# Kernel tuning notes

Measured on AMD Instinct MI355X. Metric: run time of the kernel, lower is better.

The kernel has to match this reference:

```python
import jax, jax.numpy as jnp
import numpy as np

PS = 4          # patch_size (square)
STRIDE = 2
PAD = (PS - 1) // 2
HEADS = 8
DIM = 256       # attn_dim == dim (kv_dim > dim, dim_reduc=1)
KV_DIM = 512
HD = DIM // HEADS
SCALE = HD ** -0.5
NP2 = PS * PS   # 16 elements per window


def _unfold(x, k, s, p):
    """torch.nn.functional.unfold: (B,C,H,W) -> (B, C*k*k, Ho*Wo)."""
    B, C, H, W = x.shape
    xp = jnp.pad(x, ((0, 0), (0, 0), (p, p), (p, p)))
    Ho = (H + 2 * p - k) // s + 1
    Wo = (W + 2 * p - k) // s + 1
    r = (jnp.arange(Ho) * s)[:, None] + jnp.arange(k)   # (Ho,k)
    c = (jnp.arange(Wo) * s)[:, None] + jnp.arange(k)   # (Wo,k)
    pt = xp[:, :, r][:, :, :, :, c]                     # (B,C,Ho,k,Wo,k)
    pt = pt.transpose(0, 1, 3, 5, 2, 4)                 # (B,C,k,k,Ho,Wo)
    return pt.reshape(B, C * k * k, Ho * Wo)


def _fold(y, C, Hout, Wout, k, s, p):
    """torch.nn.functional.fold: (B, C*k*k, Ho*Wo) -> (B,C,Hout,Wout), overlap-add."""
    B = y.shape[0]
    Ho = (Hout + 2 * p - k) // s + 1
    Wo = (Wout + 2 * p - k) // s + 1
    pt = y.reshape(B, C, k, k, Ho, Wo).transpose(0, 1, 4, 2, 5, 3)  # (B,C,Ho,k,Wo,k)
    r = (jnp.arange(Ho) * s)[:, None] + jnp.arange(k)
    c = (jnp.arange(Wo) * s)[:, None] + jnp.arange(k)
    out = jnp.zeros((B, C, Hout + 2 * p, Wout + 2 * p), y.dtype)
    out = out.at[:, :, r[:, :, None, None], c[None, None, :, :]].add(pt)
    return out[:, :, p:Hout + p, p:Wout + p]


def _patch_softmax(attn, Ht, Wt, Hb, Wb):
    """Normalize exp(attn) by per-bottom-pixel sums computed via a fold/unfold round trip
    (faithful to the original, including its reshape layout)."""
    a = jnp.exp(attn)                                                # (B*HtWt, H, 16, 1)
    s = a.reshape(-1, Ht * Wt, HEADS, NP2).transpose(0, 2, 3, 1)     # (B, H, 16, HtWt)
    s = s.reshape(-1, NP2, Ht * Wt)                                  # (B*H, 16, HtWt)
    s = _fold(s, 1, Hb, Wb, PS, STRIDE, PAD)                         # (B*H, 1, Hb, Wb)
    s = _unfold(s, PS, STRIDE, PAD).transpose(0, 2, 1)               # (B*H, HtWt, 16)
    s = jnp.where(s == 0, jnp.ones((), s.dtype), s)
    return a / s.reshape(-1, HEADS, NP2, 1)


def _forward(Xt, Xb, q_w, kv_w, proj_w, proj_b, rel_init, rel_bias, Ht, Wt, Hb, Wb):
    B, _, C = Xb.shape
    # im2col: gather 4x4 windows of the fine map, one window per coarse token
    Xbp = Xb.transpose(0, 2, 1).reshape(B, C, Hb, Wb)
    Xbp = _unfold(Xbp, PS, STRIDE, PAD)                              # (B, C*16, Ht*Wt)
    Xbp = Xbp.reshape(B, C, NP2, Ht * Wt).transpose(0, 3, 2, 1)
    Xbp = Xbp.reshape(B * Ht * Wt, NP2, C)                           # queries (top_down)
    Xtq = Xt.reshape(-1, 1, Xt.shape[-1])                            # (B*HtWt, 1, kv_dim)

    q = (Xbp @ q_w.T).reshape(-1, NP2, HEADS, HD).transpose(0, 2, 1, 3)  # (BHW,H,16,hd)
    kv = (Xtq @ kv_w.T).reshape(-1, 1, 2, HEADS, HD).transpose(2, 0, 3, 1, 4)
    k, v = kv[0], kv[1]                                              # (BHW,H,1,hd)

    attn = (q @ jnp.swapaxes(k, -2, -1)) * SCALE                     # (BHW,H,16,1)
    attn = attn + rel_init[:, None] + rel_bias[:, None]
    attn = _patch_softmax(attn, Ht, Wt, Hb, Wb)

    out = (attn @ v).transpose(0, 2, 1, 3).reshape(-1, NP2, DIM)     # (BHW,16,DIM)
    out = out.reshape(B, Ht * Wt, NP2, DIM).transpose(0, 3, 2, 1)
    out = out.reshape(B, DIM * NP2, Ht * Wt)
    out = _fold(out, DIM, Hb, Wb, PS, STRIDE, PAD)                   # (B,DIM,Hb,Wb)
    out = out.transpose(0, 2, 3, 1).reshape(B, Hb * Wb, DIM)
    return out @ proj_w.T + proj_b


def setup_inputs() -> dict:
    key = jax.random.key(0)
    ks = jax.random.split(key, 7)
    B, Ht, Wt, Hb, Wb = 4, 64, 64, 128, 128
    return {
        "Xt": jax.random.normal(ks[0], (B, Ht * Wt, KV_DIM), jnp.float32),
        "Xb": jax.random.normal(ks[1], (B, Hb * Wb, DIM), jnp.float32),
        "q_w": jax.random.normal(ks[2], (DIM, DIM), jnp.float32) * 0.02,
        "kv_w": jax.random.normal(ks[3], (2 * DIM, KV_DIM), jnp.float32) * 0.02,
        "proj_w": jax.random.normal(ks[4], (DIM, DIM), jnp.float32) * 0.02,
        "proj_b": jnp.zeros((DIM,), jnp.float32),
        "rel_init": jax.random.normal(ks[5], (NP2,), jnp.float32) * 0.02,
        "rel_bias": jax.random.normal(ks[6], (NP2,), jnp.float32) * 0.02,
        "Ht": Ht, "Wt": Wt, "Hb": Hb, "Wb": Wb,
    }


def reference(Xt, Xb, q_w, kv_w, proj_w, proj_b, rel_init, rel_bias, Ht, Wt, Hb, Wb):
    return _forward(Xt, Xb, q_w, kv_w, proj_w, proj_b, rel_init, rel_bias, Ht, Wt, Hb, Wb)
```

## Files before the change

### kernel.cpp

```cpp
#include <hip/hip_runtime.h>
#include <math.h>

constexpr int B_    = 4;
constexpr int HT    = 64,  WT = 64;
constexpr int HB    = 128, WB = 128;
constexpr int DIM   = 256;
constexpr int KVD   = 512;
constexpr int HEADS = 8;
constexpr int NP2   = 16;
constexpr int NPIX  = HB * WB;
constexpr int NWIN  = HT * WT;
constexpr float SCALE = 0.17677669529663687f;

using bf16x8 = __attribute__((ext_vector_type(8))) short;
using f32x4  = __attribute__((ext_vector_type(4))) float;

__device__ __forceinline__ unsigned short f2bf(float f) {
  union { float f; unsigned u; } v; v.f = f;
  unsigned r = v.u + 0x7fffu + ((v.u >> 16) & 1u);
  return (unsigned short)(r >> 16);
}

__global__ __launch_bounds__(256) void cast_bf16(
    const float* __restrict__ in, unsigned short* __restrict__ out, int n4)
{
  const int i = blockIdx.x * 256 + threadIdx.x;
  if (i >= n4) return;
  float4 v = ((const float4*)in)[i];
  ushort4 o;
  o.x = f2bf(v.x); o.y = f2bf(v.y); o.z = f2bf(v.z); o.w = f2bf(v.w);
  ((ushort4*)out)[i] = o;
}

template<bool BF16_OUT, bool BIAS>
__global__ __launch_bounds__(256) void gemm_bf16(
    const unsigned short* __restrict__ A, const unsigned short* __restrict__ Bw,
    const float* __restrict__ bias, void* __restrict__ C,
    int M, int N, int K)
{
  __shared__ unsigned short Ash[128 * 32];
  __shared__ unsigned short Bsh[128 * 32];

  const int tid  = threadIdx.x;
  const int wave = tid >> 6;
  const int lane = tid & 63;
  const int m0 = blockIdx.x * 128;
  const int n0 = blockIdx.y * 128;
  const int wm = (wave >> 1) * 64;
  const int wn = (wave & 1) * 64;

  const int c0 = wave * 64 + lane;
  const int c1 = 256 + c0;
  const int r0 = c0 >> 2, k0off = (c0 & 3) * 8;
  const int r1 = c1 >> 2, k1off = (c1 & 3) * 8;
  const int ldsOff0 = wave * 1024;
  const int ldsOff1 = 4096 + wave * 1024;

  f32x4 acc[4][4];
#pragma unroll
  for (int i = 0; i < 4; ++i)
#pragma unroll
    for (int j = 0; j < 4; ++j) { f32x4 z = {0.f, 0.f, 0.f, 0.f}; acc[i][j] = z; }

  const int fr = lane & 15;
  const int fk = (lane >> 4) * 8;

  for (int kk = 0; kk < K; kk += 32) {
    __syncthreads();
    const unsigned short* a0 = A  + (size_t)(m0 + r0) * K + kk + k0off;
    const unsigned short* a1 = A  + (size_t)(m0 + r1) * K + kk + k1off;
    const unsigned short* b0 = Bw + (size_t)(n0 + r0) * K + kk + k0off;
    const unsigned short* b1 = Bw + (size_t)(n0 + r1) * K + kk + k1off;
    __builtin_amdgcn_global_load_lds(
        (const __attribute__((address_space(1))) unsigned int*)a0,
        (__attribute__((address_space(3))) unsigned int*)((char*)Ash + ldsOff0),
        16, 0, 0);
    __builtin_amdgcn_global_load_lds(
        (const __attribute__((address_space(1))) unsigned int*)a1,
        (__attribute__((address_space(3))) unsigned int*)((char*)Ash + ldsOff1),
        16, 0, 0);
    __builtin_amdgcn_global_load_lds(
        (const __attribute__((address_space(1))) unsigned int*)b0,
        (__attribute__((address_space(3))) unsigned int*)((char*)Bsh + ldsOff0),
        16, 0, 0);
    __builtin_amdgcn_global_load_lds(
        (const __attribute__((address_space(1))) unsigned int*)b1,
        (__attribute__((address_space(3))) unsigned int*)((char*)Bsh + ldsOff1),
        16, 0, 0);
    __syncthreads();

    bf16x8 af[4], bfr[4];
#pragma unroll
    for (int t = 0; t < 4; ++t) {
      af[t]  = *(const bf16x8*)&Ash[(wm + t * 16 + fr) * 32 + fk];
      bfr[t] = *(const bf16x8*)&Bsh[(wn + t * 16 + fr) * 32 + fk];
    }
#pragma unroll
    for (int mt = 0; mt < 4; ++mt)
#pragma unroll
      for (int nt = 0; nt < 4; ++nt)
        acc[mt][nt] = __builtin_amdgcn_mfma_f32_16x16x32_bf16(
            af[mt], bfr[nt], acc[mt][nt], 0, 0, 0);
  }

  const int col0 = lane & 15;
  const int rb   = (lane >> 4) * 4;
#pragma unroll
  for (int mt = 0; mt < 4; ++mt) {
#pragma unroll
    for (int nt = 0; nt < 4; ++nt) {
      const int col = n0 + wn + nt * 16 + col0;
      float bv = BIAS ? bias[col] : 0.f;
#pragma unroll
      for (int r = 0; r < 4; ++r) {
        const int row = m0 + wm + mt * 16 + rb + r;
        const float v = acc[mt][nt][r] + bv;
        if (BF16_OUT) ((unsigned short*)C)[(size_t)row * N + col] = f2bf(v);
        else          ((float*)C)[(size_t)row * N + col] = v;
      }
    }
  }
}

__global__ __launch_bounds__(256) void e_kernel(
    const unsigned short* __restrict__ Qh, const unsigned short* __restrict__ KVh,
    const float* __restrict__ rel_init, const float* __restrict__ rel_bias,
    float* __restrict__ E)
{
  const int t   = threadIdx.x;
  const int wg  = blockIdx.x * 2 + (t >> 7);
  const int lcl = t & 127;
  const int h   = lcl >> 4, p = lcl & 15;
  const int b = wg >> 12, w = wg & 4095;
  const int i = w >> 6, j = w & 63;
  const int y = 2 * i + (p >> 2) - 1;
  const int x = 2 * j + (p & 3) - 1;

  const uint4* kp = (const uint4*)(KVh + (size_t)wg * KVD + h * 32);
  uint4 kv0 = kp[0], kv1 = kp[1], kv2 = kp[2], kv3 = kp[3];

  uint4 qv0 = {0,0,0,0}, qv1 = {0,0,0,0}, qv2 = {0,0,0,0}, qv3 = {0,0,0,0};
  if ((unsigned)y < (unsigned)HB && (unsigned)x < (unsigned)WB) {
    const uint4* qp = (const uint4*)(Qh + ((size_t)(b * NPIX + y * WB + x)) * DIM + h * 32);
    qv0 = qp[0]; qv1 = qp[1]; qv2 = qp[2]; qv3 = qp[3];
  }

  float acc = 0.f;
  const unsigned qa[16] = {qv0.x,qv0.y,qv0.z,qv0.w, qv1.x,qv1.y,qv1.z,qv1.w,
                           qv2.x,qv2.y,qv2.z,qv2.w, qv3.x,qv3.y,qv3.z,qv3.w};
  const unsigned ka[16] = {kv0.x,kv0.y,kv0.z,kv0.w, kv1.x,kv1.y,kv1.z,kv1.w,
                           kv2.x,kv2.y,kv2.z,kv2.w, kv3.x,kv3.y,kv3.z,kv3.w};
#pragma unroll
  for (int q = 0; q < 16; ++q) {
    acc = fmaf(__uint_as_float(qa[q] << 16),
               __uint_as_float(ka[q] << 16), acc);
    acc = fmaf(__uint_as_float(qa[q] & 0xffff0000u),
               __uint_as_float(ka[q] & 0xffff0000u), acc);
  }
  E[(size_t)wg * 128 + h * NP2 + p] = expf(acc * SCALE + rel_init[p] + rel_bias[p]);
}

__global__ __launch_bounds__(256) void s_kernel(
    const float* __restrict__ E, float* __restrict__ S)
{
  const int idx = blockIdx.x * 256 + threadIdx.x;
  const int b  = idx >> 17;
  const int r  = idx & 131071;
  const int h  = r >> 14;
  const int yx = r & 16383;
  const int y  = yx >> 7, x = yx & 127;

  const int ilo = max(0, (y - 1) >> 1), ihi = min(HT - 1, (y + 1) >> 1);
  const int jlo = max(0, (x - 1) >> 1), jhi = min(WT - 1, (x + 1) >> 1);

  float s = 0.f;
  for (int i = ilo; i <= ihi; ++i)
    for (int j = jlo; j <= jhi; ++j) {
      const int p = (y + 1 - 2 * i) * 4 + (x + 1 - 2 * j);
      s += E[((size_t)(b * NWIN + i * WT + j)) * 128 + h * NP2 + p];
    }
  S[idx] = s;
}

__global__ __launch_bounds__(256) void r_kernel(
    const float* __restrict__ E, const float* __restrict__ S,
    float* __restrict__ R)
{
  const int idx = blockIdx.x * 256 + threadIdx.x;
  const int b  = idx >> 19;
  const int r  = idx & 524287;
  const int w  = r >> 7;
  const int t7 = r & 127;
  const int h  = t7 >> 4, p = t7 & 15;

  const int h_eff = w >> 9;
  const int w_eff = ((w & 511) << 3) + h;
  const int i2 = w_eff >> 6, j2 = w_eff & 63;
  const int y2 = 2 * i2 + (p >> 2) - 1;
  const int x2 = 2 * j2 + (p & 3) - 1;
  float s = 1.f;
  if ((unsigned)y2 < (unsigned)HB && (unsigned)x2 < (unsigned)WB)
    s = S[(size_t)((b * HEADS + h_eff) * NPIX) + y2 * WB + x2];
  R[idx] = E[idx] / s;
}

__global__ __launch_bounds__(256) void o_kernel(
    const float* __restrict__ R, const unsigned short* __restrict__ KVh,
    unsigned short* __restrict__ out_pre)
{
  const int t  = threadIdx.x;
  const int pg = blockIdx.x * 8 + (t >> 5);
  const int b  = pg >> 14;
  const int yx = pg & 16383;
  const int y  = yx >> 7, x = yx & 127;
  const int c8 = t & 31;
  const int h  = c8 >> 2;

  const int ilo = max(0, (y - 1) >> 1), ihi = min(HT - 1, (y + 1) >> 1);
  const int jlo = max(0, (x - 1) >> 1), jhi = min(WT - 1, (x + 1) >> 1);

  float acc[8] = {};
  for (int i = ilo; i <= ihi; ++i)
    for (int j = jlo; j <= jhi; ++j) {
      const int w = i * WT + j;
      const int p = (y + 1 - 2 * i) * 4 + (x + 1 - 2 * j);
      const float rr = R[((size_t)(b * NWIN + w)) * 128 + h * NP2 + p];
      const uint4 v = *(const uint4*)(KVh + ((size_t)(b * NWIN + w)) * KVD + 256 + c8 * 8);
      const unsigned vv[4] = {v.x, v.y, v.z, v.w};
#pragma unroll
      for (int q = 0; q < 4; ++q) {
        acc[2*q]   = fmaf(rr, __uint_as_float(vv[q] << 16),        acc[2*q]);
        acc[2*q+1] = fmaf(rr, __uint_as_float(vv[q] & 0xffff0000u), acc[2*q+1]);
      }
    }

  uint4 ov;
  ov.x = (unsigned)f2bf(acc[0]) | ((unsigned)f2bf(acc[1]) << 16);
  ov.y = (unsigned)f2bf(acc[2]) | ((unsigned)f2bf(acc[3]) << 16);
  ov.z = (unsigned)f2bf(acc[4]) | ((unsigned)f2bf(acc[5]) << 16);
  ov.w = (unsigned)f2bf(acc[6]) | ((unsigned)f2bf(acc[7]) << 16);
  *(uint4*)(out_pre + (size_t)pg * DIM + c8 * 8) = ov;
}

extern "C" void kernel_launch(void* const* d_in, const int* in_sizes, int n_in,
                              void* d_out, int out_size, void* d_ws, size_t ws_size,
                              hipStream_t stream) {
  const float* Xt       = (const float*)d_in[0];
  const float* Xb       = (const float*)d_in[1];
  const float* q_w      = (const float*)d_in[2];
  const float* kv_w     = (const float*)d_in[3];
  const float* proj_w   = (const float*)d_in[4];
  const float* proj_b   = (const float*)d_in[5];
  const float* rel_init = (const float*)d_in[6];
  const float* rel_bias = (const float*)d_in[7];
  float* out = (float*)d_out;

  char* ws = (char*)d_ws;
  const size_t nXb = (size_t)B_ * NPIX * DIM;
  const size_t nXt = (size_t)B_ * NWIN * KVD;
  const size_t nQW = (size_t)DIM * DIM;
  const size_t nKVW = (size_t)KVD * KVD;
  unsigned short* Xbh  = (unsigned short*)ws;  ws += nXb * 2;
  unsigned short* Xth  = (unsigned short*)ws;  ws += nXt * 2;
  unsigned short* Qh   = (unsigned short*)ws;  ws += nXb * 2;
  unsigned short* KVh  = (unsigned short*)ws;  ws += nXt * 2;
  float*          E    = (float*)ws;           ws += (size_t)B_ * NWIN * 128 * 4;
  float*          S    = (float*)ws;           ws += (size_t)B_ * HEADS * NPIX * 4;
  unsigned short* qwh  = (unsigned short*)ws;  ws += nQW * 2;
  unsigned short* kvwh = (unsigned short*)ws;  ws += nKVW * 2;
  unsigned short* pwh  = (unsigned short*)ws;  ws += nQW * 2;
  unsigned short* Oh   = Xbh;
  float*          R    = (float*)Xth;

  const dim3 blk(256);

  cast_bf16<<<dim3((int)(nXb / 1024)), blk, 0, stream>>>(Xb, Xbh, (int)(nXb / 4));
  cast_bf16<<<dim3((int)(nXt / 1024)), blk, 0, stream>>>(Xt, Xth, (int)(nXt / 4));
  cast_bf16<<<dim3((int)(nQW / 1024)), blk, 0, stream>>>(q_w, qwh, (int)(nQW / 4));
  cast_bf16<<<dim3((int)(nKVW / 1024)), blk, 0, stream>>>(kv_w, kvwh, (int)(nKVW / 4));
  cast_bf16<<<dim3((int)(nQW / 1024)), blk, 0, stream>>>(proj_w, pwh, (int)(nQW / 4));

  gemm_bf16<true, false><<<dim3(B_ * NPIX / 128, DIM / 128), blk, 0, stream>>>(
      Xbh, qwh, nullptr, Qh, B_ * NPIX, DIM, DIM);

  gemm_bf16<true, false><<<dim3(B_ * NWIN / 128, KVD / 128), blk, 0, stream>>>(
      Xth, kvwh, nullptr, KVh, B_ * NWIN, KVD, KVD);

  e_kernel<<<dim3(B_ * NWIN / 2), blk, 0, stream>>>(Qh, KVh, rel_init, rel_bias, E);

  s_kernel<<<dim3(B_ * HEADS * NPIX / 256), blk, 0, stream>>>(E, S);

  r_kernel<<<dim3(B_ * NWIN * 128 / 256), blk, 0, stream>>>(E, S, R);

  o_kernel<<<dim3(B_ * NPIX / 8), blk, 0, stream>>>(R, KVh, Oh);

  gemm_bf16<false, true><<<dim3(B_ * NPIX / 128, DIM / 128), blk, 0, stream>>>(
      Oh, pwh, proj_b, out, B_ * NPIX, DIM, DIM);
}
```

Baseline: 278.0 us.

## Fuse casts, fold Xb cast into Q GEMM, merge score and sum kernels

Replaces five cast launches with one combined cast kernel for Xt and the weights. The Xb cast is removed by a new GEMM that loads fp32 A and converts it to bf16 while writing to LDS. The e_kernel and s_kernel are merged into a per-pixel kernel that computes the scores, writes E, and accumulates S directly. This cuts launches and intermediate traffic, but the A loads in the Q GEMM become synchronous register loads instead of global_load_lds. Each pixel kernel also re-reads K rows per window, which adds some redundant global loads.

Measured after the change: 262.0 us. -5.7%, faster.

```diff
diff --git a/kernel.cpp b/kernel.cpp
--- a/kernel.cpp
+++ b/kernel.cpp
@@ -21,22 +21,32 @@
   return (unsigned short)(r >> 16);
 }
 
-__global__ __launch_bounds__(256) void cast_bf16(
-    const float* __restrict__ in, unsigned short* __restrict__ out, int n4)
+constexpr int NXT4  = B_ * NWIN * KVD / 4;
+constexpr int NQW4  = DIM * DIM / 4;
+constexpr int NKVW4 = KVD * KVD / 4;
+constexpr int NCAST4 = NXT4 + NQW4 + NKVW4 + NQW4;
+
+__global__ __launch_bounds__(256) void cast_all(
+    const float* __restrict__ Xt, const float* __restrict__ qw,
+    const float* __restrict__ kvw, const float* __restrict__ pw,
+    unsigned short* __restrict__ Xth, unsigned short* __restrict__ qwh,
+    unsigned short* __restrict__ kvwh, unsigned short* __restrict__ pwh)
 {
   const int i = blockIdx.x * 256 + threadIdx.x;
-  if (i >= n4) return;
-  float4 v = ((const float4*)in)[i];
+  const float* src; unsigned short* dst; int off;
+  if (i < NXT4)                     { src = Xt;  dst = Xth;  off = i; }
+  else if (i < NXT4 + NQW4)         { src = qw;  dst = qwh;  off = i - NXT4; }
+  else if (i < NXT4 + NQW4 + NKVW4) { src = kvw; dst = kvwh; off = i - NXT4 - NQW4; }
+  else                              { src = pw;  dst = pwh;  off = i - NXT4 - NQW4 - NKVW4; }
+  float4 v = ((const float4*)src)[off];
   ushort4 o;
   o.x = f2bf(v.x); o.y = f2bf(v.y); o.z = f2bf(v.z); o.w = f2bf(v.w);
-  ((ushort4*)out)[i] = o;
-}
-
-template<bool BF16_OUT, bool BIAS>
-__global__ __launch_bounds__(256) void gemm_bf16(
-    const unsigned short* __restrict__ A, const unsigned short* __restrict__ Bw,
-    const float* __restrict__ bias, void* __restrict__ C,
-    int M, int N, int K)
+  ((ushort4*)dst)[off] = o;
+}
+
+__global__ __launch_bounds__(256) void gemm_af32(
+    const float* __restrict__ A, const unsigned short* __restrict__ Bw,
+    unsigned short* __restrict__ C, int M, int N, int K)
 {
   __shared__ unsigned short Ash[128 * 32];
   __shared__ unsigned short Bsh[128 * 32];
@@ -67,6 +77,93 @@
 
   for (int kk = 0; kk < K; kk += 32) {
     __syncthreads();
+#pragma unroll
+    for (int u = 0; u < 4; ++u) {
+      const int c   = tid + u * 256;
+      const int row = c >> 3;
+      const int kq  = (c & 7) * 4;
+      float4 v = *(const float4*)(A + (size_t)(m0 + row) * K + kk + kq);
+      uint2 pk;
+      pk.x = (unsigned)f2bf(v.x) | ((unsigned)f2bf(v.y) << 16);
+      pk.y = (unsigned)f2bf(v.z) | ((unsigned)f2bf(v.w) << 16);
+      *(uint2*)&Ash[row * 32 + kq] = pk;
+    }
+    const unsigned short* b0 = Bw + (size_t)(n0 + r0) * K + kk + k0off;
+    const unsigned short* b1 = Bw + (size_t)(n0 + r1) * K + kk + k1off;
+    __builtin_amdgcn_global_load_lds(
+        (const __attribute__((address_space(1))) unsigned int*)b0,
+        (__attribute__((address_space(3))) unsigned int*)((char*)Bsh + ldsOff0),
+        16, 0, 0);
+    __builtin_amdgcn_global_load_lds(
+        (const __attribute__((address_space(1))) unsigned int*)b1,
+        (__attribute__((address_space(3))) unsigned int*)((char*)Bsh + ldsOff1),
+        16, 0, 0);
+    __syncthreads();
+
+    bf16x8 af[4], bfr[4];
+#pragma unroll
+    for (int t = 0; t < 4; ++t) {
+      af[t]  = *(const bf16x8*)&Ash[(wm + t * 16 + fr) * 32 + fk];
+      bfr[t] = *(const bf16x8*)&Bsh[(wn + t * 16 + fr) * 32 + fk];
+    }
+#pragma unroll
+    for (int mt = 0; mt < 4; ++mt)
+#pragma unroll
+      for (int nt = 0; nt < 4; ++nt)
+        acc[mt][nt] = __builtin_amdgcn_mfma_f32_16x16x32_bf16(
+            af[mt], bfr[nt], acc[mt][nt], 0, 0, 0);
+  }
+
+  const int col0 = lane & 15;
+  const int rb   = (lane >> 4) * 4;
+#pragma unroll
+  for (int mt = 0; mt < 4; ++mt)
+#pragma unroll
+    for (int nt = 0; nt < 4; ++nt) {
+      const int col = n0 + wn + nt * 16 + col0;
+#pragma unroll
+      for (int r = 0; r < 4; ++r) {
+        const int row = m0 + wm + mt * 16 + rb + r;
+        C[(size_t)row * N + col] = f2bf(acc[mt][nt][r]);
+      }
+    }
+}
+
+template<bool BF16_OUT, bool BIAS>
+__global__ __launch_bounds__(256) void gemm_bf16(
+    const unsigned short* __restrict__ A, const unsigned short* __restrict__ Bw,
+    const float* __restrict__ bias, void* __restrict__ C,
+    int M, int N, int K)
+{
+  __shared__ unsigned short Ash[128 * 32];
+  __shared__ unsigned short Bsh[128 * 32];
+
+  const int tid  = threadIdx.x;
+  const int wave = tid >> 6;
+  const int lane = tid & 63;
+  const int m0 = blockIdx.x * 128;
+  const int n0 = blockIdx.y * 128;
+  const int wm = (wave >> 1) * 64;
+  const int wn = (wave & 1) * 64;
+
+  const int c0 = wave * 64 + lane;
+  const int c1 = 256 + c0;
+  const int r0 = c0 >> 2, k0off = (c0 & 3) * 8;
+  const int r1 = c1 >> 2, k1off = (c1 & 3) * 8;
+  const int ldsOff0 = wave * 1024;
+  const int ldsOff1 = 4096 + wave * 1024;
+
+  f32x4 acc[4][4];
+#pragma unroll
+  for (int i = 0; i < 4; ++i)
+#pragma unroll
+    for (int j = 0; j < 4; ++j) { f32x4 z = {0.f, 0.f, 0.f, 0.f}; acc[i][j] = z; }
+
+  const int fr = lane & 15;
+  const int fk = (lane >> 4) * 8;
+
+  for (int kk = 0; kk < K; kk += 32) {
+    __syncthreads();
     const unsigned short* a0 = A  + (size_t)(m0 + r0) * K + kk + k0off;
     const unsigned short* a1 = A  + (size_t)(m0 + r1) * K + kk + k1off;
     const unsigned short* b0 = Bw + (size_t)(n0 + r0) * K + kk + k0off;
@@ -106,7 +203,7 @@
   const int col0 = lane & 15;
   const int rb   = (lane >> 4) * 4;
 #pragma unroll
-  for (int mt = 0; mt < 4; ++mt) {
+  for (int mt = 0; mt < 4; ++mt)
 #pragma unroll
     for (int nt = 0; nt < 4; ++nt) {
       const int col = n0 + wn + nt * 16 + col0;
@@ -119,56 +216,23 @@
         else          ((float*)C)[(size_t)row * N + col] = v;
       }
     }
-  }
-}
-
-__global__ __launch_bounds__(256) void e_kernel(
+}
+
+__global__ __launch_bounds__(256) void es_kernel(
     const unsigned short* __restrict__ Qh, const unsigned short* __restrict__ KVh,
     const float* __restrict__ rel_init, const float* __restrict__ rel_bias,
-    float* __restrict__ E)
-{
-  const int t   = threadIdx.x;
-  const int wg  = blockIdx.x * 2 + (t >> 7);
-  const int lcl = t & 127;
-  const int h   = lcl >> 4, p = lcl & 15;
-  const int b = wg >> 12, w = wg & 4095;
-  const int i = w >> 6, j = w & 63;
-  const int y = 2 * i + (p >> 2) - 1;
-  const int x = 2 * j + (p & 3) - 1;
-
-  const uint4* kp = (const uint4*)(KVh + (size_t)wg * KVD + h * 32);
-  uint4 kv0 = kp[0], kv1 = kp[1], kv2 = kp[2], kv3 = kp[3];
-
-  uint4 qv0 = {0,0,0,0}, qv1 = {0,0,0,0}, qv2 = {0,0,0,0}, qv3 = {0,0,0,0};
-  if ((unsigned)y < (unsigned)HB && (unsigned)x < (unsigned)WB) {
-    const uint4* qp = (const uint4*)(Qh + ((size_t)(b * NPIX + y * WB + x)) * DIM + h * 32);
-    qv0 = qp[0]; qv1 = qp[1]; qv2 = qp[2]; qv3 = qp[3];
-  }
-
-  float acc = 0.f;
-  const unsigned qa[16] = {qv0.x,qv0.y,qv0.z,qv0.w, qv1.x,qv1.y,qv1.z,qv1.w,
-                           qv2.x,qv2.y,qv2.z,qv2.w, qv3.x,qv3.y,qv3.z,qv3.w};
-  const unsigned ka[16] = {kv0.x,kv0.y,kv0.z,kv0.w, kv1.x,kv1.y,kv1.z,kv1.w,
-                           kv2.x,kv2.y,kv2.z,kv2.w, kv3.x,kv3.y,kv3.z,kv3.w};
-#pragma unroll
-  for (int q = 0; q < 16; ++q) {
-    acc = fmaf(__uint_as_float(qa[q] << 16),
-               __uint_as_float(ka[q] << 16), acc);
-    acc = fmaf(__uint_as_float(qa[q] & 0xffff0000u),
-               __uint_as_float(ka[q] & 0xffff0000u), acc);
-  }
-  E[(size_t)wg * 128 + h * NP2 + p] = expf(acc * SCALE + rel_init[p] + rel_bias[p]);
-}
-
-__global__ __launch_bounds__(256) void s_kernel(
-    const float* __restrict__ E, float* __restrict__ S)
+    float* __restrict__ E, float* __restrict__ S)
 {
   const int idx = blockIdx.x * 256 + threadIdx.x;
-  const int b  = idx >> 17;
-  const int r  = idx & 131071;
-  const int h  = r >> 14;
-  const int yx = r & 16383;
-  const int y  = yx >> 7, x = yx & 127;
+  const int h = idx & 7;
+  const int x = (idx >> 3) & 127;
+  const int y = (idx >> 10) & 127;
+  const int b = idx >> 17;
+
+  const uint4* qp = (const uint4*)(Qh + ((size_t)((b << 14) + y * WB + x)) * DIM + h * 32);
+  uint4 q0 = qp[0], q1 = qp[1], q2 = qp[2], q3 = qp[3];
+  const unsigned qa[16] = {q0.x,q0.y,q0.z,q0.w, q1.x,q1.y,q1.z,q1.w,
+                           q2.x,q2.y,q2.z,q2.w, q3.x,q3.y,q3.z,q3.w};
 
   const int ilo = max(0, (y - 1) >> 1), ihi = min(HT - 1, (y + 1) >> 1);
   const int jlo = max(0, (x - 1) >> 1), jhi = min(WT - 1, (x + 1) >> 1);
@@ -176,10 +240,25 @@
   float s = 0.f;
   for (int i = ilo; i <= ihi; ++i)
     for (int j = jlo; j <= jhi; ++j) {
+      const int w = i * WT + j;
       const int p = (y + 1 - 2 * i) * 4 + (x + 1 - 2 * j);
-      s += E[((size_t)(b * NWIN + i * WT + j)) * 128 + h * NP2 + p];
-    }
-  S[idx] = s;
+      const uint4* kp = (const uint4*)(KVh + ((size_t)((b << 12) + w)) * KVD + h * 32);
+      uint4 k0 = kp[0], k1 = kp[1], k2 = kp[2], k3 = kp[3];
+      const unsigned ka[16] = {k0.x,k0.y,k0.z,k0.w, k1.x,k1.y,k1.z,k1.w,
+                               k2.x,k2.y,k2.z,k2.w, k3.x,k3.y,k3.z,k3.w};
+      float acc = 0.f;
+#pragma unroll
+      for (int q = 0; q < 16; ++q) {
+        acc = fmaf(__uint_as_float(qa[q] << 16),
+                   __uint_as_float(ka[q] << 16), acc);
+        acc = fmaf(__uint_as_float(qa[q] & 0xffff0000u),
+                   __uint_as_float(ka[q] & 0xffff0000u), acc);
+      }
+      const float e = expf(acc * SCALE + rel_init[p] + rel_bias[p]);
+      E[((size_t)((b << 12) + w)) * 128 + h * NP2 + p] = e;
+      s += e;
+    }
+  S[(size_t)((b * HEADS + h) << 14) + y * WB + x] = s;
 }
 
 __global__ __launch_bounds__(256) void r_kernel(
@@ -229,7 +308,7 @@
       const unsigned vv[4] = {v.x, v.y, v.z, v.w};
 #pragma unroll
       for (int q = 0; q < 4; ++q) {
-        acc[2*q]   = fmaf(rr, __uint_as_float(vv[q] << 16),        acc[2*q]);
+        acc[2*q]   = fmaf(rr, __uint_as_float(vv[q] << 16),         acc[2*q]);
         acc[2*q+1] = fmaf(rr, __uint_as_float(vv[q] & 0xffff0000u), acc[2*q+1]);
       }
     }
@@ -260,35 +339,30 @@
   const size_t nXt = (size_t)B_ * NWIN * KVD;
   const size_t nQW = (size_t)DIM * DIM;
   const size_t nKVW = (size_t)KVD * KVD;
-  unsigned short* Xbh  = (unsigned short*)ws;  ws += nXb * 2;
+  unsigned short* Qh   = (unsigned short*)ws;  ws += nXb * 2;
   unsigned short* Xth  = (unsigned short*)ws;  ws += nXt * 2;
-  unsigned short* Qh   = (unsigned short*)ws;  ws += nXb * 2;
   unsigned short* KVh  = (unsigned short*)ws;  ws += nXt * 2;
   float*          E    = (float*)ws;           ws += (size_t)B_ * NWIN * 128 * 4;
   float*          S    = (float*)ws;           ws += (size_t)B_ * HEADS * NPIX * 4;
   unsigned short* qwh  = (unsigned short*)ws;  ws += nQW * 2;
   unsigned short* kvwh = (unsigned short*)ws;  ws += nKVW * 2;
   unsigned short* pwh  = (unsigned short*)ws;  ws += nQW * 2;
-  unsigned short* Oh   = Xbh;
   float*          R    = (float*)Xth;
+  unsigned short* Oh   = Qh;
 
   const dim3 blk(256);
 
-  cast_bf16<<<dim3((int)(nXb / 1024)), blk, 0, stream>>>(Xb, Xbh, (int)(nXb / 4));
-  cast_bf16<<<dim3((int)(nXt / 1024)), blk, 0, stream>>>(Xt, Xth, (int)(nXt / 4));
-  cast_bf16<<<dim3((int)(nQW / 1024)), blk, 0, stream>>>(q_w, qwh, (int)(nQW / 4));
-  cast_bf16<<<dim3((int)(nKVW / 1024)), blk, 0, stream>>>(kv_w, kvwh, (int)(nKVW / 4));
-  cast_bf16<<<dim3((int)(nQW / 1024)), blk, 0, stream>>>(proj_w, pwh, (int)(nQW / 4));
-
-  gemm_bf16<true, false><<<dim3(B_ * NPIX / 128, DIM / 128), blk, 0, stream>>>(
-      Xbh, qwh, nullptr, Qh, B_ * NPIX, DIM, DIM);
+  cast_all<<<dim3(NCAST4 / 256), blk, 0, stream>>>(
+      Xt, q_w, kv_w, proj_w, Xth, qwh, kvwh, pwh);
+
+  gemm_af32<<<dim3(B_ * NPIX / 128, DIM / 128), blk, 0, stream>>>(
+      Xb, qwh, Qh, B_ * NPIX, DIM, DIM);
 
   gemm_bf16<true, false><<<dim3(B_ * NWIN / 128, KVD / 128), blk, 0, stream>>>(
       Xth, kvwh, nullptr, KVh, B_ * NWIN, KVD, KVD);
 
-  e_kernel<<<dim3(B_ * NWIN / 2), blk, 0, stream>>>(Qh, KVh, rel_init, rel_bias, E);
-
-  s_kernel<<<dim3(B_ * HEADS * NPIX / 256), blk, 0, stream>>>(E, S);
+  es_kernel<<<dim3(B_ * NPIX * HEADS / 256), blk, 0, stream>>>(
+      Qh, KVh, rel_init, rel_bias, E, S);
 
   r_kernel<<<dim3(B_ * NWIN * 128 / 256), blk, 0, stream>>>(E, S, R);
 
```
